# Performance work log

Measured on AMD Instinct MI355X. Metric: run time of the kernel, lower is better.

The kernel has to match this reference:

```python
import jax, jax.numpy as jnp
import numpy as np

N_REV, N_USER, N_ITEM, DEG, D = 100000, 4096, 4096, 16, 64
HID = 128

def setup_inputs() -> dict:
    key = jax.random.key(0)
    ks = jax.random.split(key, 9)
    return {
        "review_vecs": jax.random.normal(ks[0], (N_REV, D), jnp.float32),
        "user_vecs": jax.random.normal(ks[1], (N_USER, D), jnp.float32),
        "item_vecs": jax.random.normal(ks[2], (N_ITEM, D), jnp.float32),
        "user_weights": jax.random.normal(ks[3], (DEG * 2 * D, HID), jnp.float32) * 0.05,
        "item_weights": jax.random.normal(ks[4], (DEG * 2 * D, HID), jnp.float32) * 0.05,
        "adj0": jax.random.randint(ks[5], (N_USER, DEG), 0, N_REV, jnp.int32),
        "adj1": jax.random.randint(ks[6], (N_USER, DEG), 0, N_ITEM, jnp.int32),
        "adj2": jax.random.randint(ks[7], (N_ITEM, DEG), 0, N_REV, jnp.int32),
        "adj3": jax.random.randint(ks[8], (N_ITEM, DEG), 0, N_USER, jnp.int32),
    }

def _sdpa(q, k, v):
    # dense scaled dot-product attention: q,k [N,d], v [N,F]
    scale = 1.0 / jnp.sqrt(jnp.asarray(q.shape[-1], q.dtype))
    w = jax.nn.softmax(jnp.einsum('nd,md->nm', q, k) * scale, axis=-1)
    return jnp.einsum('nm,mf->nf', w, v)

def reference(review_vecs, user_vecs, item_vecs, user_weights, item_weights,
              adj0, adj1, adj2, adj3):
    # dropout=0.0 -> identity; feature-dim shuffle is random augmentation,
    # replaced by identity permutation for a deterministic reference.
    ur = review_vecs[adj0]           # [Nu, deg, D]
    ri = item_vecs[adj1]             # [Nu, deg, D]
    ir = review_vecs[adj2]           # [Ni, deg, D]
    ru = user_vecs[adj3]             # [Ni, deg, D]
    cu = jnp.concatenate([ur, ri], axis=2).reshape(adj0.shape[0], -1)  # [Nu, deg*2D]
    ci = jnp.concatenate([ir, ru], axis=2).reshape(adj2.shape[0], -1)  # [Ni, deg*2D]
    cu = _sdpa(user_vecs, user_vecs, cu)
    ci = _sdpa(item_vecs, item_vecs, ci)
    user_out = jax.nn.relu(cu @ user_weights)   # [Nu, HID]
    item_out = jax.nn.relu(ci @ item_weights)   # [Ni, HID]
    return user_out, item_out
```

## Files before the change

### kernel.cpp

```cpp
#include <hip/hip_runtime.h>
#include <hip/hip_bf16.h>
#include <math.h>

#define N_NODES 4096
#define N_REV 100000
#define DEG 16
#define DIM 64
#define HID 128

typedef __attribute__((ext_vector_type(8))) short bf16x8;
typedef __attribute__((ext_vector_type(4))) float f32x4;
typedef __attribute__((ext_vector_type(16))) float f32x16;

static __device__ __forceinline__ unsigned pk2(float a, float b) {
    __hip_bfloat162 h = __float22bfloat162_rn(make_float2(a, b));
    return *reinterpret_cast<unsigned*>(&h);
}

static __device__ __forceinline__ void gl_lds16(const void* g, void* l) {
    __builtin_amdgcn_global_load_lds(
        (const __attribute__((address_space(1))) unsigned int*)g,
        (__attribute__((address_space(3))) unsigned int*)l, 16, 0, 0);
}

__global__ __launch_bounds__(256)
void prep_all(const float* __restrict__ U, const float* __restrict__ I,
              const float* __restrict__ uW, const float* __restrict__ iW,
              ushort* __restrict__ Ub, ushort* __restrict__ Ib,
              ushort* __restrict__ wt)
{
    __shared__ float wt_f[64 * 128];
    const int t = threadIdx.x;
    if (blockIdx.x < 256) {
        int i = blockIdx.x * 256 + t;
        const float* src; ushort* dst; int j;
        if (i < 32768) { src = U; dst = Ub; j = i; }
        else           { src = I; dst = Ib; j = i - 32768; }
        float4 a = ((const float4*)src)[j * 2];
        float4 b = ((const float4*)src)[j * 2 + 1];
        uint4 o;
        o.x = pk2(a.x, a.y); o.y = pk2(a.z, a.w);
        o.z = pk2(b.x, b.y); o.w = pk2(b.z, b.w);
        ((uint4*)dst)[j] = o;
        return;
    }
    const int b = blockIdx.x - 256;
    const int side = b >> 5, kc = b & 31;
    const float* __restrict__ W = side ? iW : uW;
    const float4* src = (const float4*)(W + (size_t)kc * 64 * 128);
    #pragma unroll
    for (int j = 0; j < 8; ++j)
        ((float4*)wt_f)[j * 256 + t] = src[j * 256 + t];
    __syncthreads();
    #pragma unroll
    for (int j = 0; j < 4; ++j) {
        int c = j * 256 + t;
        int h = c >> 3, seg = c & 7;
        int sp = seg ^ (h & 7);
        float v[8];
        #pragma unroll
        for (int jj = 0; jj < 8; ++jj) v[jj] = wt_f[(sp * 8 + jj) * 128 + h];
        uint4 o;
        o.x = pk2(v[0], v[1]); o.y = pk2(v[2], v[3]);
        o.z = pk2(v[4], v[5]); o.w = pk2(v[6], v[7]);
        *(uint4*)(wt + ((size_t)(side * 32 + kc) * 1024 + c) * 8) = o;
    }
}

#define GB_STRIDE 16384
#define GADJ_OFF  32768

__global__ __launch_bounds__(256)
void gemm_gather(const float* __restrict__ review,
                 const float* __restrict__ userv,
                 const float* __restrict__ itemv,
                 const ushort* __restrict__ wt,
                 const int* __restrict__ adj0, const int* __restrict__ adj1,
                 const int* __restrict__ adj2, const int* __restrict__ adj3,
                 ushort* __restrict__ vprojT)
{
    const int side = blockIdx.x >> 8, rem = blockIdx.x & 255;
    const int tile = rem >> 1, hb = rem & 1;
    const int* __restrict__ adjA = side ? adj2 : adj0;
    const int* __restrict__ adjB = side ? adj3 : adj1;
    const float* __restrict__ vecB = side ? userv : itemv;
    const ushort* __restrict__ wbase = wt + (size_t)side * 32 * 8192;
    ushort* __restrict__ outT = vprojT + (size_t)side * HID * N_NODES;

    __shared__ __align__(16) char smem[36864];
    int* adjs = (int*)(smem + GADJ_OFF);
    const int t = threadIdx.x;
    const int w = t >> 6, lane = t & 63;
    const int wm = w >> 1, wn = w & 1;
    const int g = lane >> 4, qi = lane & 15;
    const int swz = (qi & 7) << 4;

    if (t < 128)
        ((int4*)adjs)[t] = ((const int4*)(adjA + tile * 512))[t];
    else
        ((int4*)adjs)[t] = ((const int4*)(adjB + tile * 512))[t - 128];
    __syncthreads();

    f32x4 acc[2];
    #pragma unroll
    for (int i = 0; i < 2; ++i) acc[i] = f32x4{0.f, 0.f, 0.f, 0.f};

    auto stage = [&](int kc, int b) {
        const int d = kc >> 1, half = kc & 1;
        char* base = smem + b * GB_STRIDE;
        const float* vs = half ? vecB : review;
        #pragma unroll
        for (int j = 0; j < 2; ++j) {
            int c = j * 256 + t;
            int row = c >> 4, seg = c & 15;
            int idx = adjs[half * 512 + row * 16 + d];
            gl_lds16(vs + (size_t)idx * 64 + (seg ^ (row & 7)) * 4,
                     base + (c >> 6) * 1024);
        }
        const ushort* wsrc = wbase + (size_t)kc * 8192;
        #pragma unroll
        for (int j = 0; j < 2; ++j) {
            int c = j * 256 + t;
            gl_lds16(wsrc + (size_t)(hb * 512 + c) * 8,
                     base + 8192 + (c >> 6) * 1024);
        }
    };

    stage(0, 0);
    __syncthreads();

    for (int kc = 0; kc < 32; ++kc) {
        const int cur = kc & 1;
        if (kc < 31) stage(kc + 1, cur ^ 1);

        const char* cb = smem + cur * GB_STRIDE;
        const int ab0 = (wm * 16 + qi) * 256 + g * 32;
        f32x4 af0 = *(const f32x4*)(cb + ((ab0)       ^ swz));
        f32x4 af1 = *(const f32x4*)(cb + ((ab0 + 16)  ^ swz));
        f32x4 af2 = *(const f32x4*)(cb + ((ab0 + 128) ^ swz));
        f32x4 af3 = *(const f32x4*)(cb + ((ab0 + 144) ^ swz));
        union { unsigned u[4]; bf16x8 s; } A0, A1;
        A0.u[0] = pk2(af0[0], af0[1]); A0.u[1] = pk2(af0[2], af0[3]);
        A0.u[2] = pk2(af1[0], af1[1]); A0.u[3] = pk2(af1[2], af1[3]);
        A1.u[0] = pk2(af2[0], af2[1]); A1.u[1] = pk2(af2[2], af2[3]);
        A1.u[2] = pk2(af3[0], af3[1]); A1.u[3] = pk2(af3[2], af3[3]);

        #pragma unroll
        for (int nf = 0; nf < 2; ++nf) {
            int bbase = 8192 + (wn * 32 + nf * 16 + qi) * 128 + g * 16;
            bf16x8 b0 = *(const bf16x8*)(cb + ((bbase)      ^ swz));
            bf16x8 b1 = *(const bf16x8*)(cb + ((bbase + 64) ^ swz));
            acc[nf] = __builtin_amdgcn_mfma_f32_16x16x32_bf16(A0.s, b0, acc[nf], 0, 0, 0);
            acc[nf] = __builtin_amdgcn_mfma_f32_16x16x32_bf16(A1.s, b1, acc[nf], 0, 0, 0);
        }
        __syncthreads();
    }

    #pragma unroll
    for (int nf = 0; nf < 2; ++nf) {
        int h = hb * 64 + wn * 32 + nf * 16 + qi;
        uint2 p;
        p.x = pk2(acc[nf][0], acc[nf][1]);
        p.y = pk2(acc[nf][2], acc[nf][3]);
        *(uint2*)(outT + (size_t)h * N_NODES + tile * 32 + wm * 16 + g * 4) = p;
    }
}

#define FSTRIDE 24576

__global__ __launch_bounds__(256, 2)
void flash_attn_mfma(const float* __restrict__ userv,
                     const float* __restrict__ itemv,
                     const ushort* __restrict__ Ub,
                     const ushort* __restrict__ Ib,
                     const ushort* __restrict__ vprojT,
                     ushort* __restrict__ po,
                     float* __restrict__ pl)
{
    const int side = blockIdx.x >> 8;
    const int rem  = blockIdx.x & 255;
    const int qb   = rem >> 3;
    const int kvb  = rem & 7;
    const float* __restrict__ X = side ? itemv : userv;
    const ushort* __restrict__ Xb = side ? Ib : Ub;
    const ushort* __restrict__ V = vprojT + (size_t)side * HID * N_NODES;
    const int part = side * 8 + kvb;

    __shared__ __align__(16) char smem[49152];

    const int t = threadIdx.x;
    const int w = t >> 6, lane = t & 63;
    const int col = lane & 31, h5 = lane >> 5;
    const int q0 = qb * 128 + w * 32;

    bf16x8 qf[4];
    {
        const float* qp = X + (size_t)(q0 + col) * DIM;
        #pragma unroll
        for (int ks = 0; ks < 4; ++ks) {
            int d0 = ks * 16 + h5 * 8;
            float4 v0 = *(const float4*)(qp + d0);
            float4 v1 = *(const float4*)(qp + d0 + 4);
            union { unsigned u[4]; bf16x8 s; } rr;
            rr.u[0] = pk2(v0.x * 0.125f, v0.y * 0.125f);
            rr.u[1] = pk2(v0.z * 0.125f, v0.w * 0.125f);
            rr.u[2] = pk2(v1.x * 0.125f, v1.y * 0.125f);
            rr.u[3] = pk2(v1.z * 0.125f, v1.w * 0.125f);
            qf[ks] = rr.s;
        }
    }

    const f32x16 z16 = {0.f,0.f,0.f,0.f, 0.f,0.f,0.f,0.f,
                        0.f,0.f,0.f,0.f, 0.f,0.f,0.f,0.f};
    f32x16 o[4];
    #pragma unroll
    for (int ht = 0; ht < 4; ++ht) o[ht] = z16;
    float psum = 0.f;

    auto stage = [&](int it, int b) {
        const int k0 = kvb * 512 + it * 64;
        char* base = smem + b * FSTRIDE;
        #pragma unroll
        for (int j = 0; j < 2; ++j) {
            int c = j * 256 + t;
            int row = c >> 3, seg = c & 7;
            gl_lds16(Xb + (size_t)(k0 + row) * 64 + (seg ^ (row & 7)) * 8,
                     base + (c >> 6) * 1024);
        }
        #pragma unroll
        for (int j = 0; j < 4; ++j) {
            int c = j * 256 + t;
            int hh = c >> 3, seg = c & 7;
            gl_lds16(V + (size_t)hh * N_NODES + k0 + (seg ^ (hh & 7)) * 8,
                     base + 8192 + (c >> 6) * 1024);
        }
    };

    stage(0, 0);
    __syncthreads();

    for (int it = 0; it < 8; ++it) {
        const int cur = it & 1;
        if (it < 7) stage(it + 1, cur ^ 1);
        const char* kb = smem + cur * FSTRIDE;
        const char* vt = kb + 8192;

        #pragma unroll
        for (int T = 0; T < 2; ++T) {
            f32x16 s = z16;
            #pragma unroll
            for (int ks = 0; ks < 4; ++ks) {
                int row = T * 32 + col;
                int abase = (row * 128 + ks * 32 + h5 * 16) ^ ((row & 7) << 4);
                bf16x8 ka = *(const bf16x8*)(kb + abase);
                s = __builtin_amdgcn_mfma_f32_32x32x16_bf16(ka, qf[ks], s, 0, 0, 0);
            }
            float p[16];
            #pragma unroll
            for (int r = 0; r < 16; ++r) {
                p[r] = __expf(s[r]);
                psum += p[r];
            }
            #pragma unroll
            for (int win = 0; win < 2; ++win) {
                unsigned ca0 = pk2(p[win*8 + 0], p[win*8 + 1]);
                unsigned ca1 = pk2(p[win*8 + 2], p[win*8 + 3]);
                unsigned cb0 = pk2(p[win*8 + 4], p[win*8 + 5]);
                unsigned cb1 = pk2(p[win*8 + 6], p[win*8 + 7]);
                asm volatile("v_permlane32_swap_b32 %0, %1"
                             : "+v"(ca0), "+v"(cb0));
                asm volatile("v_permlane32_swap_b32 %0, %1"
                             : "+v"(ca1), "+v"(cb1));
                union { unsigned u[4]; bf16x8 s8; } pa;
                pa.u[0] = ca0; pa.u[1] = ca1; pa.u[2] = cb0; pa.u[3] = cb1;
                #pragma unroll
                for (int ht = 0; ht < 4; ++ht) {
                    int hrow = ht * 32 + col;
                    int vbase = (hrow * 128 + T * 64 + win * 32 + h5 * 16)
                                ^ ((hrow & 7) << 4);
                    bf16x8 vb = *(const bf16x8*)(vt + vbase);
                    o[ht] = __builtin_amdgcn_mfma_f32_32x32x16_bf16(pa.s8, vb, o[ht], 0, 0, 0);
                }
            }
        }
        __syncthreads();
    }

    float pt = psum + __shfl_xor(psum, 32);
    if (lane < 32)
        pl[(size_t)part * N_NODES + q0 + col] = pt;

    ushort* pob = po + (size_t)part * N_NODES * HID;
    #pragma unroll
    for (int ht = 0; ht < 4; ++ht)
        #pragma unroll
        for (int r = 0; r < 16; ++r) {
            int q = q0 + (r & 3) + 8 * (r >> 2) + 4 * h5;
            pob[(size_t)q * HID + ht * 32 + col] =
                (ushort)(pk2(o[ht][r], 0.f) & 0xffffu);
        }
}

__global__ __launch_bounds__(256)
void merge_parts(const ushort* __restrict__ po, const float* __restrict__ pl,
                 float* __restrict__ out)
{
    int idx = blockIdx.x * 256 + threadIdx.x;
    int side = idx >> 18;
    int q    = (idx >> 6) & 4095;
    int h2   = idx & 63;
    float sx = 0.f, sy = 0.f, l = 0.f;
    #pragma unroll
    for (int p = 0; p < 8; ++p) {
        int part = side * 8 + p;
        unsigned v = *(const unsigned*)(po + (size_t)part * (N_NODES * HID)
                                           + q * HID + h2 * 2);
        union { unsigned u; float f; } lo, hi;
        lo.u = v << 16; hi.u = v & 0xffff0000u;
        sx += lo.f; sy += hi.f;
        l += pl[(size_t)part * N_NODES + q];
    }
    float li = 1.0f / l;
    float2 r = make_float2(fmaxf(sx * li, 0.f), fmaxf(sy * li, 0.f));
    ((float2*)out)[idx] = r;
}

extern "C" void kernel_launch(void* const* d_in, const int* in_sizes, int n_in,
                              void* d_out, int out_size, void* d_ws, size_t ws_size,
                              hipStream_t stream)
{
    const float* review = (const float*)d_in[0];
    const float* userv  = (const float*)d_in[1];
    const float* itemv  = (const float*)d_in[2];
    const float* uW     = (const float*)d_in[3];
    const float* iW     = (const float*)d_in[4];
    const int*   adj0   = (const int*)d_in[5];
    const int*   adj1   = (const int*)d_in[6];
    const int*   adj2   = (const int*)d_in[7];
    const int*   adj3   = (const int*)d_in[8];
    float* out = (float*)d_out;

    char* ws = (char*)d_ws;
    char* ob = (char*)d_out;
    float*  pl     = (float*)ws;
    ushort* po     = (ushort*)(ws + 262144);
    ushort* wt     = (ushort*)(ws + 262144);
    ushort* vprojT = (ushort*)(ob);
    ushort* Ub     = (ushort*)(ob + 2097152);
    ushort* Ib     = (ushort*)(ob + 2621440);

    prep_all<<<320, 256, 0, stream>>>(userv, itemv, uW, iW, Ub, Ib, wt);
    gemm_gather<<<512, 256, 0, stream>>>(review, userv, itemv, wt,
                                         adj0, adj1, adj2, adj3, vprojT);
    flash_attn_mfma<<<512, 256, 0, stream>>>(userv, itemv, Ub, Ib, vprojT,
                                             po, pl);
    merge_parts<<<2048, 256, 0, stream>>>(po, pl, out);
}
```

Before: 56.64 us.

## Fuse merge into attention via atomic tickets and restructure gather GEMM tiling

Removes the separate merge_parts launch. The last of the eight KV-partition blocks for each query block, picked with an atomic ticket counter, now does the normalize and ReLU merge itself. The gather GEMM also changes: each block now covers the full 128-wide HID with a 32x32x16 MFMA instead of two 64-wide halves, which halves the grid and avoids gathering the same rows twice. Gathered A rows are loaded into registers, converted to bf16 and written to LDS instead of going to LDS as fp32. Workspace buffers move out of the output into the workspace, trading a kernel launch for threadfence and atomic overhead plus a serialized tail merge.

```diff
diff --git a/kernel.cpp b/kernel.cpp
--- a/kernel.cpp
+++ b/kernel.cpp
@@ -27,7 +27,7 @@
 void prep_all(const float* __restrict__ U, const float* __restrict__ I,
               const float* __restrict__ uW, const float* __restrict__ iW,
               ushort* __restrict__ Ub, ushort* __restrict__ Ib,
-              ushort* __restrict__ wt)
+              ushort* __restrict__ wt, int* __restrict__ cnt)
 {
     __shared__ float wt_f[64 * 128];
     const int t = threadIdx.x;
@@ -44,6 +44,7 @@
         ((uint4*)dst)[j] = o;
         return;
     }
+    if (blockIdx.x == 256 && t < 64) cnt[t] = 0;
     const int b = blockIdx.x - 256;
     const int side = b >> 5, kc = b & 31;
     const float* __restrict__ W = side ? iW : uW;
@@ -67,8 +68,8 @@
     }
 }
 
-#define GB_STRIDE 16384
-#define GADJ_OFF  32768
+#define GSTRIDE 20480
+#define GADJ    40960
 
 __global__ __launch_bounds__(256)
 void gemm_gather(const float* __restrict__ review,
@@ -79,21 +80,19 @@
                  const int* __restrict__ adj2, const int* __restrict__ adj3,
                  ushort* __restrict__ vprojT)
 {
-    const int side = blockIdx.x >> 8, rem = blockIdx.x & 255;
-    const int tile = rem >> 1, hb = rem & 1;
+    const int side = blockIdx.x >> 7, tile = blockIdx.x & 127;
     const int* __restrict__ adjA = side ? adj2 : adj0;
     const int* __restrict__ adjB = side ? adj3 : adj1;
     const float* __restrict__ vecB = side ? userv : itemv;
     const ushort* __restrict__ wbase = wt + (size_t)side * 32 * 8192;
     ushort* __restrict__ outT = vprojT + (size_t)side * HID * N_NODES;
 
-    __shared__ __align__(16) char smem[36864];
-    int* adjs = (int*)(smem + GADJ_OFF);
+    __shared__ __align__(16) char smem[45056];
+    int* adjs = (int*)(smem + GADJ);
     const int t = threadIdx.x;
-    const int w = t >> 6, lane = t & 63;
-    const int wm = w >> 1, wn = w & 1;
-    const int g = lane >> 4, qi = lane & 15;
-    const int swz = (qi & 7) << 4;
+    const int wn = t >> 6, lane = t & 63;
+    const int col = lane & 31, h5 = lane >> 5;
+    const int arow = t >> 3, aseg = t & 7;
 
     if (t < 128)
         ((int4*)adjs)[t] = ((const int4*)(adjA + tile * 512))[t];
@@ -101,68 +100,65 @@
         ((int4*)adjs)[t] = ((const int4*)(adjB + tile * 512))[t - 128];
     __syncthreads();
 
-    f32x4 acc[2];
-    #pragma unroll
-    for (int i = 0; i < 2; ++i) acc[i] = f32x4{0.f, 0.f, 0.f, 0.f};
-
-    auto stage = [&](int kc, int b) {
+    const f32x16 z16 = {0.f,0.f,0.f,0.f, 0.f,0.f,0.f,0.f,
+                        0.f,0.f,0.f,0.f, 0.f,0.f,0.f,0.f};
+    f32x16 acc = z16;
+    float4 a0, a1;
+
+    auto issueW = [&](int kc, int b) {
+        const ushort* ws_ = wbase + (size_t)kc * 8192;
+        #pragma unroll
+        for (int j = 0; j < 4; ++j)
+            gl_lds16(ws_ + (size_t)(j * 256 + t) * 8,
+                     smem + b * GSTRIDE + 4096 + j * 4096 + (t >> 6) * 1024);
+    };
+    auto issueA = [&](int kc) {
         const int d = kc >> 1, half = kc & 1;
-        char* base = smem + b * GB_STRIDE;
         const float* vs = half ? vecB : review;
-        #pragma unroll
-        for (int j = 0; j < 2; ++j) {
-            int c = j * 256 + t;
-            int row = c >> 4, seg = c & 15;
-            int idx = adjs[half * 512 + row * 16 + d];
-            gl_lds16(vs + (size_t)idx * 64 + (seg ^ (row & 7)) * 4,
-                     base + (c >> 6) * 1024);
-        }
-        const ushort* wsrc = wbase + (size_t)kc * 8192;
-        #pragma unroll
-        for (int j = 0; j < 2; ++j) {
-            int c = j * 256 + t;
-            gl_lds16(wsrc + (size_t)(hb * 512 + c) * 8,
-                     base + 8192 + (c >> 6) * 1024);
-        }
+        int idx = adjs[half * 512 + arow * 16 + d];
+        const float* p = vs + (size_t)idx * 64 + aseg * 8;
+        a0 = *(const float4*)p; a1 = *(const float4*)(p + 4);
     };
-
-    stage(0, 0);
-    __syncthreads();
-
+    auto writeA = [&](int b) {
+        uint4 pk;
+        pk.x = pk2(a0.x, a0.y); pk.y = pk2(a0.z, a0.w);
+        pk.z = pk2(a1.x, a1.y); pk.w = pk2(a1.z, a1.w);
+        *(uint4*)(smem + b * GSTRIDE +
+                  ((arow * 128 + aseg * 16) ^ ((arow & 7) << 4))) = pk;
+    };
+
+    issueW(0, 0); issueA(0); writeA(0);
+    __syncthreads();
+
+    const int hq = wn * 32 + col;
     for (int kc = 0; kc < 32; ++kc) {
         const int cur = kc & 1;
-        if (kc < 31) stage(kc + 1, cur ^ 1);
-
-        const char* cb = smem + cur * GB_STRIDE;
-        const int ab0 = (wm * 16 + qi) * 256 + g * 32;
-        f32x4 af0 = *(const f32x4*)(cb + ((ab0)       ^ swz));
-        f32x4 af1 = *(const f32x4*)(cb + ((ab0 + 16)  ^ swz));
-        f32x4 af2 = *(const f32x4*)(cb + ((ab0 + 128) ^ swz));
-        f32x4 af3 = *(const f32x4*)(cb + ((ab0 + 144) ^ swz));
-        union { unsigned u[4]; bf16x8 s; } A0, A1;
-        A0.u[0] = pk2(af0[0], af0[1]); A0.u[1] = pk2(af0[2], af0[3]);
-        A0.u[2] = pk2(af1[0], af1[1]); A0.u[3] = pk2(af1[2], af1[3]);
-        A1.u[0] = pk2(af2[0], af2[1]); A1.u[1] = pk2(af2[2], af2[3]);
-        A1.u[2] = pk2(af3[0], af3[1]); A1.u[3] = pk2(af3[2], af3[3]);
-
-        #pragma unroll
-        for (int nf = 0; nf < 2; ++nf) {
-            int bbase = 8192 + (wn * 32 + nf * 16 + qi) * 128 + g * 16;
-            bf16x8 b0 = *(const bf16x8*)(cb + ((bbase)      ^ swz));
-            bf16x8 b1 = *(const bf16x8*)(cb + ((bbase + 64) ^ swz));
-            acc[nf] = __builtin_amdgcn_mfma_f32_16x16x32_bf16(A0.s, b0, acc[nf], 0, 0, 0);
-            acc[nf] = __builtin_amdgcn_mfma_f32_16x16x32_bf16(A1.s, b1, acc[nf], 0, 0, 0);
-        }
+        if (kc < 31) { issueW(kc + 1, cur ^ 1); issueA(kc + 1); }
+
+        const char* cb = smem + cur * GSTRIDE;
+        bf16x8 ka[4], wb[4];
+        #pragma unroll
+        for (int ks = 0; ks < 4; ++ks) {
+            ka[ks] = *(const bf16x8*)(cb +
+                ((col * 128 + ks * 32 + h5 * 16) ^ ((col & 7) << 4)));
+            wb[ks] = *(const bf16x8*)(cb + 4096 +
+                ((hq * 128 + ks * 32 + h5 * 16) ^ ((hq & 7) << 4)));
+        }
+        #pragma unroll
+        for (int ks = 0; ks < 4; ++ks)
+            acc = __builtin_amdgcn_mfma_f32_32x32x16_bf16(ka[ks], wb[ks], acc, 0, 0, 0);
+
+        if (kc < 31) writeA(cur ^ 1);
         __syncthreads();
     }
 
     #pragma unroll
-    for (int nf = 0; nf < 2; ++nf) {
-        int h = hb * 64 + wn * 32 + nf * 16 + qi;
-        uint2 p;
-        p.x = pk2(acc[nf][0], acc[nf][1]);
-        p.y = pk2(acc[nf][2], acc[nf][3]);
-        *(uint2*)(outT + (size_t)h * N_NODES + tile * 32 + wm * 16 + g * 4) = p;
+    for (int rp = 0; rp < 4; ++rp) {
+        uint2 pv;
+        pv.x = pk2(acc[rp * 4 + 0], acc[rp * 4 + 1]);
+        pv.y = pk2(acc[rp * 4 + 2], acc[rp * 4 + 3]);
+        int node = tile * 32 + 8 * rp + 4 * h5;
+        *(uint2*)(outT + (size_t)hq * N_NODES + node) = pv;
     }
 }
 
@@ -175,7 +171,9 @@
                      const ushort* __restrict__ Ib,
                      const ushort* __restrict__ vprojT,
                      ushort* __restrict__ po,
-                     float* __restrict__ pl)
+                     float* __restrict__ pl,
+                     int* __restrict__ cnt,
+                     float* __restrict__ out)
 {
     const int side = blockIdx.x >> 8;
     const int rem  = blockIdx.x & 255;
@@ -187,6 +185,7 @@
     const int part = side * 8 + kvb;
 
     __shared__ __align__(16) char smem[49152];
+    __shared__ int ticket;
 
     const int t = threadIdx.x;
     const int w = t >> 6, lane = t & 63;
@@ -299,30 +298,35 @@
             pob[(size_t)q * HID + ht * 32 + col] =
                 (ushort)(pk2(o[ht][r], 0.f) & 0xffffu);
         }
-}
-
-__global__ __launch_bounds__(256)
-void merge_parts(const ushort* __restrict__ po, const float* __restrict__ pl,
-                 float* __restrict__ out)
-{
-    int idx = blockIdx.x * 256 + threadIdx.x;
-    int side = idx >> 18;
-    int q    = (idx >> 6) & 4095;
-    int h2   = idx & 63;
-    float sx = 0.f, sy = 0.f, l = 0.f;
-    #pragma unroll
-    for (int p = 0; p < 8; ++p) {
-        int part = side * 8 + p;
-        unsigned v = *(const unsigned*)(po + (size_t)part * (N_NODES * HID)
-                                           + q * HID + h2 * 2);
-        union { unsigned u; float f; } lo, hi;
-        lo.u = v << 16; hi.u = v & 0xffff0000u;
-        sx += lo.f; sy += hi.f;
-        l += pl[(size_t)part * N_NODES + q];
-    }
-    float li = 1.0f / l;
-    float2 r = make_float2(fmaxf(sx * li, 0.f), fmaxf(sy * li, 0.f));
-    ((float2*)out)[idx] = r;
+
+    __threadfence();
+    __syncthreads();
+    if (t == 0) ticket = atomicAdd(cnt + side * 32 + qb, 1);
+    __syncthreads();
+    if (ticket != 7) return;
+    __threadfence();
+
+    const int gq0 = qb * 128;
+    const int h2u = t & 63;
+    const int qsub = t >> 6;
+    #pragma unroll 4
+    for (int pass = 0; pass < 32; ++pass) {
+        int q = gq0 + pass * 4 + qsub;
+        float sx = 0.f, sy = 0.f, l = 0.f;
+        #pragma unroll
+        for (int p = 0; p < 8; ++p) {
+            int pp = side * 8 + p;
+            unsigned v = *(const unsigned*)(po + (size_t)pp * (N_NODES * HID)
+                                               + (size_t)q * HID + h2u * 2);
+            union { unsigned u; float f; } lo, hi;
+            lo.u = v << 16; hi.u = v & 0xffff0000u;
+            sx += lo.f; sy += hi.f;
+            l += pl[(size_t)pp * N_NODES + q];
+        }
+        float li = 1.0f / l;
+        float2 r = make_float2(fmaxf(sx * li, 0.f), fmaxf(sy * li, 0.f));
+        ((float2*)out)[((size_t)side * N_NODES + q) * 64 + h2u] = r;
+    }
 }
 
 extern "C" void kernel_launch(void* const* d_in, const int* in_sizes, int n_in,
@@ -341,18 +345,17 @@
     float* out = (float*)d_out;
 
     char* ws = (char*)d_ws;
-    char* ob = (char*)d_out;
-    float*  pl     = (float*)ws;
-    ushort* po     = (ushort*)(ws + 262144);
-    ushort* wt     = (ushort*)(ws + 262144);
-    ushort* vprojT = (ushort*)(ob);
-    ushort* Ub     = (ushort*)(ob + 2097152);
-    ushort* Ib     = (ushort*)(ob + 2621440);
-
-    prep_all<<<320, 256, 0, stream>>>(userv, itemv, uW, iW, Ub, Ib, wt);
-    gemm_gather<<<512, 256, 0, stream>>>(review, userv, itemv, wt,
+    float*  pl     = (float*)(ws + 0x000000);
+    int*    cnt    = (int*)  (ws + 0x040000);
+    ushort* wt     = (ushort*)(ws + 0x080000);
+    ushort* vprojT = (ushort*)(ws + 0x180000);
+    ushort* Ub     = (ushort*)(ws + 0x380000);
+    ushort* Ib     = (ushort*)(ws + 0x400000);
+    ushort* po     = (ushort*)(ws + 0x480000);
+
+    prep_all<<<320, 256, 0, stream>>>(userv, itemv, uW, iW, Ub, Ib, wt, cnt);
+    gemm_gather<<<256, 256, 0, stream>>>(review, userv, itemv, wt,
                                          adj0, adj1, adj2, adj3, vprojT);
     flash_attn_mfma<<<512, 256, 0, stream>>>(userv, itemv, Ub, Ib, vprojT,
-                                             po, pl);
-    merge_parts<<<2048, 256, 0, stream>>>(po, pl, out);
-}
+                                             po, pl, cnt, out);
+}
```

Measured after the change: 137.5 us. +142.7%, slower.

## Drop LDS staging in flash attention, split KV into 16 parts

Applied to the files above, without the earlier changes.

The flash attention kernel no longer stages K and V tiles through double-buffered shared memory. Each wave now loads its MFMA operands straight from global memory, which removes the per-iteration barriers. The KV range is split into 16 partitions instead of 8, so the grid doubles to 1024 blocks, and launch bounds now target 4 blocks per SM. The cost is that merge_parts must read twice as many partial outputs, and the direct global loads are uncoalesced and repeated across waves, relying on cache; workspace buffers were also moved out of the output buffer.

```diff
diff --git a/kernel.cpp b/kernel.cpp
--- a/kernel.cpp
+++ b/kernel.cpp
@@ -166,9 +166,7 @@
     }
 }
 
-#define FSTRIDE 24576
-
-__global__ __launch_bounds__(256, 2)
+__global__ __launch_bounds__(256, 4)
 void flash_attn_mfma(const float* __restrict__ userv,
                      const float* __restrict__ itemv,
                      const ushort* __restrict__ Ub,
@@ -177,16 +175,14 @@
                      ushort* __restrict__ po,
                      float* __restrict__ pl)
 {
-    const int side = blockIdx.x >> 8;
-    const int rem  = blockIdx.x & 255;
-    const int qb   = rem >> 3;
-    const int kvb  = rem & 7;
+    const int side = blockIdx.x >> 9;
+    const int rem  = blockIdx.x & 511;
+    const int qb   = rem >> 4;
+    const int kvb  = rem & 15;
     const float* __restrict__ X = side ? itemv : userv;
     const ushort* __restrict__ Xb = side ? Ib : Ub;
     const ushort* __restrict__ V = vprojT + (size_t)side * HID * N_NODES;
-    const int part = side * 8 + kvb;
-
-    __shared__ __align__(16) char smem[49152];
+    const int part = side * 16 + kvb;
 
     const int t = threadIdx.x;
     const int w = t >> 6, lane = t & 63;
@@ -217,42 +213,17 @@
     for (int ht = 0; ht < 4; ++ht) o[ht] = z16;
     float psum = 0.f;
 
-    auto stage = [&](int it, int b) {
-        const int k0 = kvb * 512 + it * 64;
-        char* base = smem + b * FSTRIDE;
-        #pragma unroll
-        for (int j = 0; j < 2; ++j) {
-            int c = j * 256 + t;
-            int row = c >> 3, seg = c & 7;
-            gl_lds16(Xb + (size_t)(k0 + row) * 64 + (seg ^ (row & 7)) * 8,
-                     base + (c >> 6) * 1024);
-        }
-        #pragma unroll
-        for (int j = 0; j < 4; ++j) {
-            int c = j * 256 + t;
-            int hh = c >> 3, seg = c & 7;
-            gl_lds16(V + (size_t)hh * N_NODES + k0 + (seg ^ (hh & 7)) * 8,
-                     base + 8192 + (c >> 6) * 1024);
-        }
-    };
-
-    stage(0, 0);
-    __syncthreads();
-
-    for (int it = 0; it < 8; ++it) {
-        const int cur = it & 1;
-        if (it < 7) stage(it + 1, cur ^ 1);
-        const char* kb = smem + cur * FSTRIDE;
-        const char* vt = kb + 8192;
+    for (int it = 0; it < 4; ++it) {
+        const int k0 = kvb * 256 + it * 64;
 
         #pragma unroll
         for (int T = 0; T < 2; ++T) {
+            const int krow = k0 + T * 32 + col;
             f32x16 s = z16;
             #pragma unroll
             for (int ks = 0; ks < 4; ++ks) {
-                int row = T * 32 + col;
-                int abase = (row * 128 + ks * 32 + h5 * 16) ^ ((row & 7) << 4);
-                bf16x8 ka = *(const bf16x8*)(kb + abase);
+                bf16x8 ka = *(const bf16x8*)(Xb + (size_t)krow * 64
+                                                + ks * 16 + h5 * 8);
                 s = __builtin_amdgcn_mfma_f32_32x32x16_bf16(ka, qf[ks], s, 0, 0, 0);
             }
             float p[16];
@@ -273,17 +244,15 @@
                              : "+v"(ca1), "+v"(cb1));
                 union { unsigned u[4]; bf16x8 s8; } pa;
                 pa.u[0] = ca0; pa.u[1] = ca1; pa.u[2] = cb0; pa.u[3] = cb1;
+                const int kcol = k0 + T * 32 + win * 16 + h5 * 8;
                 #pragma unroll
                 for (int ht = 0; ht < 4; ++ht) {
-                    int hrow = ht * 32 + col;
-                    int vbase = (hrow * 128 + T * 64 + win * 32 + h5 * 16)
-                                ^ ((hrow & 7) << 4);
-                    bf16x8 vb = *(const bf16x8*)(vt + vbase);
+                    bf16x8 vb = *(const bf16x8*)(V + (size_t)(ht * 32 + col)
+                                                     * N_NODES + kcol);
                     o[ht] = __builtin_amdgcn_mfma_f32_32x32x16_bf16(pa.s8, vb, o[ht], 0, 0, 0);
                 }
             }
         }
-        __syncthreads();
     }
 
     float pt = psum + __shfl_xor(psum, 32);
@@ -311,8 +280,8 @@
     int h2   = idx & 63;
     float sx = 0.f, sy = 0.f, l = 0.f;
     #pragma unroll
-    for (int p = 0; p < 8; ++p) {
-        int part = side * 8 + p;
+    for (int p = 0; p < 16; ++p) {
+        int part = side * 16 + p;
         unsigned v = *(const unsigned*)(po + (size_t)part * (N_NODES * HID)
                                            + q * HID + h2 * 2);
         union { unsigned u; float f; } lo, hi;
@@ -341,18 +310,17 @@
     float* out = (float*)d_out;
 
     char* ws = (char*)d_ws;
-    char* ob = (char*)d_out;
-    float*  pl     = (float*)ws;
-    ushort* po     = (ushort*)(ws + 262144);
-    ushort* wt     = (ushort*)(ws + 262144);
-    ushort* vprojT = (ushort*)(ob);
-    ushort* Ub     = (ushort*)(ob + 2097152);
-    ushort* Ib     = (ushort*)(ob + 2621440);
+    float*  pl     = (float*)(ws + 0x000000);
+    ushort* wt     = (ushort*)(ws + 0x080000);
+    ushort* vprojT = (ushort*)(ws + 0x180000);
+    ushort* Ub     = (ushort*)(ws + 0x380000);
+    ushort* Ib     = (ushort*)(ws + 0x400000);
+    ushort* po     = (ushort*)(ws + 0x480000);
 
     prep_all<<<320, 256, 0, stream>>>(userv, itemv, uW, iW, Ub, Ib, wt);
     gemm_gather<<<512, 256, 0, stream>>>(review, userv, itemv, wt,
                                          adj0, adj1, adj2, adj3, vprojT);
-    flash_attn_mfma<<<512, 256, 0, stream>>>(userv, itemv, Ub, Ib, vprojT,
-                                             po, pl);
+    flash_attn_mfma<<<1024, 256, 0, stream>>>(userv, itemv, Ub, Ib, vprojT,
+                                              po, pl);
     merge_parts<<<2048, 256, 0, stream>>>(po, pl, out);
 }
```

Result: slower. 89.51 us (+58.0%).

## Move bf16 casts into gather GEMM, shrink prep kernel, reorder attention blocks

Applied to the files above, without the earlier changes.

The fp32-to-bf16 conversion of user and item vectors moves out of the prep kernel and into 256 extra blocks appended to the gather GEMM launch. The prep kernel now only transposes and converts the weights with 64 blocks, which shortens the critical path before the GEMM. The attention kernel's block index mapping is reordered so the side and KV-partition vary fastest, interleaving both sides across CUs. Workspace buffers are moved out of the output buffer into separate non-overlapping workspace regions.

```diff
diff --git a/kernel.cpp b/kernel.cpp
--- a/kernel.cpp
+++ b/kernel.cpp
@@ -24,18 +24,52 @@
 }
 
 __global__ __launch_bounds__(256)
-void prep_all(const float* __restrict__ U, const float* __restrict__ I,
-              const float* __restrict__ uW, const float* __restrict__ iW,
-              ushort* __restrict__ Ub, ushort* __restrict__ Ib,
-              ushort* __restrict__ wt)
+void prep_w(const float* __restrict__ uW, const float* __restrict__ iW,
+            ushort* __restrict__ wt)
 {
     __shared__ float wt_f[64 * 128];
     const int t = threadIdx.x;
-    if (blockIdx.x < 256) {
-        int i = blockIdx.x * 256 + t;
+    const int side = blockIdx.x >> 5, kc = blockIdx.x & 31;
+    const float* __restrict__ W = side ? iW : uW;
+    const float4* src = (const float4*)(W + (size_t)kc * 64 * 128);
+    #pragma unroll
+    for (int j = 0; j < 8; ++j)
+        ((float4*)wt_f)[j * 256 + t] = src[j * 256 + t];
+    __syncthreads();
+    #pragma unroll
+    for (int j = 0; j < 4; ++j) {
+        int c = j * 256 + t;
+        int h = c >> 3, seg = c & 7;
+        int sp = seg ^ (h & 7);
+        float v[8];
+        #pragma unroll
+        for (int jj = 0; jj < 8; ++jj) v[jj] = wt_f[(sp * 8 + jj) * 128 + h];
+        uint4 o;
+        o.x = pk2(v[0], v[1]); o.y = pk2(v[2], v[3]);
+        o.z = pk2(v[4], v[5]); o.w = pk2(v[6], v[7]);
+        *(uint4*)(wt + ((size_t)(side * 32 + kc) * 1024 + c) * 8) = o;
+    }
+}
+
+#define GB_STRIDE 16384
+#define GADJ_OFF  32768
+
+__global__ __launch_bounds__(256)
+void gemm_gather(const float* __restrict__ review,
+                 const float* __restrict__ userv,
+                 const float* __restrict__ itemv,
+                 const ushort* __restrict__ wt,
+                 const int* __restrict__ adj0, const int* __restrict__ adj1,
+                 const int* __restrict__ adj2, const int* __restrict__ adj3,
+                 ushort* __restrict__ vprojT,
+                 ushort* __restrict__ Ub, ushort* __restrict__ Ib)
+{
+    const int t = threadIdx.x;
+    if (blockIdx.x >= 512) {
+        int i = (blockIdx.x - 512) * 256 + t;
         const float* src; ushort* dst; int j;
-        if (i < 32768) { src = U; dst = Ub; j = i; }
-        else           { src = I; dst = Ib; j = i - 32768; }
+        if (i < 32768) { src = userv; dst = Ub; j = i; }
+        else           { src = itemv; dst = Ib; j = i - 32768; }
         float4 a = ((const float4*)src)[j * 2];
         float4 b = ((const float4*)src)[j * 2 + 1];
         uint4 o;
@@ -44,41 +78,7 @@
         ((uint4*)dst)[j] = o;
         return;
     }
-    const int b = blockIdx.x - 256;
-    const int side = b >> 5, kc = b & 31;
-    const float* __restrict__ W = side ? iW : uW;
-    const float4* src = (const float4*)(W + (size_t)kc * 64 * 128);
-    #pragma unroll
-    for (int j = 0; j < 8; ++j)
-        ((float4*)wt_f)[j * 256 + t] = src[j * 256 + t];
-    __syncthreads();
-    #pragma unroll
-    for (int j = 0; j < 4; ++j) {
-        int c = j * 256 + t;
-        int h = c >> 3, seg = c & 7;
-        int sp = seg ^ (h & 7);
-        float v[8];
-        #pragma unroll
-        for (int jj = 0; jj < 8; ++jj) v[jj] = wt_f[(sp * 8 + jj) * 128 + h];
-        uint4 o;
-        o.x = pk2(v[0], v[1]); o.y = pk2(v[2], v[3]);
-        o.z = pk2(v[4], v[5]); o.w = pk2(v[6], v[7]);
-        *(uint4*)(wt + ((size_t)(side * 32 + kc) * 1024 + c) * 8) = o;
-    }
-}
-
-#define GB_STRIDE 16384
-#define GADJ_OFF  32768
-
-__global__ __launch_bounds__(256)
-void gemm_gather(const float* __restrict__ review,
-                 const float* __restrict__ userv,
-                 const float* __restrict__ itemv,
-                 const ushort* __restrict__ wt,
-                 const int* __restrict__ adj0, const int* __restrict__ adj1,
-                 const int* __restrict__ adj2, const int* __restrict__ adj3,
-                 ushort* __restrict__ vprojT)
-{
+
     const int side = blockIdx.x >> 8, rem = blockIdx.x & 255;
     const int tile = rem >> 1, hb = rem & 1;
     const int* __restrict__ adjA = side ? adj2 : adj0;
@@ -89,7 +89,6 @@
 
     __shared__ __align__(16) char smem[36864];
     int* adjs = (int*)(smem + GADJ_OFF);
-    const int t = threadIdx.x;
     const int w = t >> 6, lane = t & 63;
     const int wm = w >> 1, wn = w & 1;
     const int g = lane >> 4, qi = lane & 15;
@@ -177,10 +176,10 @@
                      ushort* __restrict__ po,
                      float* __restrict__ pl)
 {
-    const int side = blockIdx.x >> 8;
-    const int rem  = blockIdx.x & 255;
-    const int qb   = rem >> 3;
-    const int kvb  = rem & 7;
+    const int grp  = blockIdx.x & 15;
+    const int side = grp >> 3;
+    const int kvb  = grp & 7;
+    const int qb   = blockIdx.x >> 4;
     const float* __restrict__ X = side ? itemv : userv;
     const ushort* __restrict__ Xb = side ? Ib : Ub;
     const ushort* __restrict__ V = vprojT + (size_t)side * HID * N_NODES;
@@ -341,17 +340,17 @@
     float* out = (float*)d_out;
 
     char* ws = (char*)d_ws;
-    char* ob = (char*)d_out;
-    float*  pl     = (float*)ws;
-    ushort* po     = (ushort*)(ws + 262144);
-    ushort* wt     = (ushort*)(ws + 262144);
-    ushort* vprojT = (ushort*)(ob);
-    ushort* Ub     = (ushort*)(ob + 2097152);
-    ushort* Ib     = (ushort*)(ob + 2621440);
-
-    prep_all<<<320, 256, 0, stream>>>(userv, itemv, uW, iW, Ub, Ib, wt);
-    gemm_gather<<<512, 256, 0, stream>>>(review, userv, itemv, wt,
-                                         adj0, adj1, adj2, adj3, vprojT);
+    float*  pl     = (float*)(ws + 0x000000);
+    ushort* wt     = (ushort*)(ws + 0x080000);
+    ushort* vprojT = (ushort*)(ws + 0x180000);
+    ushort* Ub     = (ushort*)(ws + 0x380000);
+    ushort* Ib     = (ushort*)(ws + 0x400000);
+    ushort* po     = (ushort*)(ws + 0x480000);
+
+    prep_w<<<64, 256, 0, stream>>>(uW, iW, wt);
+    gemm_gather<<<768, 256, 0, stream>>>(review, userv, itemv, wt,
+                                         adj0, adj1, adj2, adj3, vprojT,
+                                         Ub, Ib);
     flash_attn_mfma<<<512, 256, 0, stream>>>(userv, itemv, Ub, Ib, vprojT,
                                              po, pl);
     merge_parts<<<2048, 256, 0, stream>>>(po, pl, out);
```

Measured after the change: 55.82 us (median of 2 runs). About the same (-1.5%).
